# Kernel tuning notes

Measured on AMD Instinct MI355X. Metric: run time of the kernel, lower is better.

Reference implementation:

```python
import jax, jax.numpy as jnp
import numpy as np


def _bev_grid(theta, shift, H_out, W_out):
    # grid resolution in meters per output pixel (0.05 when H_out=800)
    gr = 0.05 * (800.0 / H_out)
    xs = -10.0 + gr / 2.0 + gr * jnp.arange(W_out, dtype=jnp.float32)   # [W]
    ys = 46.0 - gr / 2.0 - gr * jnp.arange(H_out, dtype=jnp.float32)    # [H]
    bx = jnp.broadcast_to(xs[None, :], (H_out, W_out))
    by = jnp.broadcast_to(ys[:, None], (H_out, W_out))
    base = jnp.stack([bx, by, jnp.ones((H_out, W_out), jnp.float32)], axis=-1)  # [H,W,3]
    # bmm(base.view(N,HW,3), theta^T) == einsum over last axis
    g = jnp.einsum('hwk,nik->nhwi', base, theta)  # [N,H,W,3]
    g = g / g[..., 2:3]
    gx = g[..., 0] / 608.0 - 1.0
    gy = (g[..., 1] - shift[:, None, None]) / 144.0 - 1.0
    return jnp.stack([gx, gy], axis=-1)  # [N,H,W,2]


def _grid_sample_bilinear_border(x, grid):
    # align_corners=False (torch default), padding_mode='border'
    N, C, Hin, Win = x.shape
    Hout, Wout = grid.shape[1], grid.shape[2]
    ix = ((grid[..., 0] + 1.0) * Win - 1.0) * 0.5
    iy = ((grid[..., 1] + 1.0) * Hin - 1.0) * 0.5
    ix0 = jnp.floor(ix)
    iy0 = jnp.floor(iy)
    wx = ix - ix0  # fractional weights
    wy = iy - iy0
    x0 = jnp.clip(ix0, 0, Win - 1).astype(jnp.int32)
    x1 = jnp.clip(ix0 + 1, 0, Win - 1).astype(jnp.int32)
    y0 = jnp.clip(iy0, 0, Hin - 1).astype(jnp.int32)
    y1 = jnp.clip(iy0 + 1, 0, Hin - 1).astype(jnp.int32)

    flat = x.reshape(N, C, Hin * Win)

    def gather(yi, xi):
        idx = (yi * Win + xi).reshape(N, 1, Hout * Wout)
        idx = jnp.broadcast_to(idx, (N, C, Hout * Wout))
        return jnp.take_along_axis(flat, idx, axis=2).reshape(N, C, Hout, Wout)

    v00 = gather(y0, x0)
    v01 = gather(y0, x1)
    v10 = gather(y1, x0)
    v11 = gather(y1, x1)
    wx = wx[:, None, :, :]
    wy = wy[:, None, :, :]
    return (v00 * (1 - wx) * (1 - wy) + v01 * wx * (1 - wy)
            + v10 * (1 - wx) * wy + v11 * wx * wy)


def setup_inputs() -> dict:
    key = jax.random.key(0)
    k1, k2, k3 = jax.random.split(key, 3)
    N, C, Hin, Win = 4, 16, 288, 1216
    x = jax.random.normal(k1, (N, C, Hin, Win), dtype=jnp.float32)
    # realistic homography: identity plus small perturbation
    theta = jnp.eye(3, dtype=jnp.float32)[None] + 0.1 * jax.random.normal(k2, (N, 3, 3), dtype=jnp.float32)
    shift = 10.0 * jax.random.uniform(k3, (N,), dtype=jnp.float32)
    return {"x": x, "theta": theta, "shift": shift, "H_out": 800, "W_out": 400}


def reference(x, theta, shift, H_out, W_out):
    grid = _bev_grid(theta, shift, H_out, W_out)
    return _grid_sample_bilinear_border(x, grid)
```

## Files before the change

kernel.cpp:

```cpp
#include <hip/hip_runtime.h>
#include <math.h>

constexpr int N    = 4;
constexpr int C    = 16;
constexpr int Hin  = 288;
constexpr int Win  = 1216;
constexpr int Hout = 800;
constexpr int Wout = 400;
constexpr int PIX_PER_N = Hout * Wout;
constexpr int CH_STRIDE = Hin * Win;

typedef float v2f __attribute__((ext_vector_type(2)));

constexpr double grd = 0.05 * (800.0 / (double)Hout);
constexpr float  GR  = (float)grd;
constexpr float  CX0 = (float)(-10.0 + grd / 2.0);
constexpr float  CY0 = (float)( 46.0 - grd / 2.0);

__device__ __forceinline__ float fbar(float x) {
    asm volatile("" : "+v"(x));
    return x;
}

struct Samp {
    int   lb0, lb1;
    bool  hi0, hi1, xpair;
    float w00, w01, w10, w11;
};

__device__ __forceinline__ Samp px_chain(int w, int h, const float* th, float shn) {
    float bx = CX0 + fbar(GR * (float)w);
    float by = CY0 - fbar(GR * (float)h);

    float t00 = th[0], t01 = th[1], t02 = th[2];
    float t10 = th[3], t11 = th[4], t12 = th[5];
    float t20 = th[6], t21 = th[7], t22 = th[8];

    float g0 = fbar(__builtin_fmaf(by, t01, fbar(bx * t00))) + t02;
    float g1 = fbar(__builtin_fmaf(by, t11, fbar(bx * t10))) + t12;
    float g2 = fbar(__builtin_fmaf(by, t21, fbar(bx * t20))) + t22;

    float p0 = g0 / g2;
    float p1 = g1 / g2;

    float gx = fbar(p0 / 608.0f) - 1.0f;
    float gy = fbar((p1 - shn) / 144.0f) - 1.0f;

    float ix = (fbar((gx + 1.0f) * (float)Win) - 1.0f) * 0.5f;
    float iy = (fbar((gy + 1.0f) * (float)Hin) - 1.0f) * 0.5f;

    float ix0f = floorf(ix);
    float iy0f = floorf(iy);
    float wx = ix - ix0f;
    float wy = iy - iy0f;

    int x0 = (int)fminf(fmaxf(ix0f,        0.0f), (float)(Win - 1));
    int x1 = (int)fminf(fmaxf(ix0f + 1.0f, 0.0f), (float)(Win - 1));
    int y0 = (int)fminf(fmaxf(iy0f,        0.0f), (float)(Hin - 1));
    int y1 = (int)fminf(fmaxf(iy0f + 1.0f, 0.0f), (float)(Hin - 1));

    float omwx = 1.0f - wx;
    float omwy = 1.0f - wy;

    Samp s;
    s.w00 = omwx * omwy;
    s.w01 = wx * omwy;
    s.w10 = omwx * wy;
    s.w11 = wx * wy;

    int lo0 = y0 * Win + x0;
    int lo1 = y1 * Win + x0;
    s.lb0 = min(lo0, CH_STRIDE - 2);
    s.lb1 = min(lo1, CH_STRIDE - 2);
    s.hi0 = lo0 > s.lb0;
    s.hi1 = lo1 > s.lb1;
    s.xpair = x1 > x0;
    return s;
}

__device__ __forceinline__ float combine(v2f r0, v2f r1, const Samp& s) {
    float v00 = s.hi0   ? r0.y : r0.x;
    float v01 = s.xpair ? r0.y : v00;
    float v10 = s.hi1   ? r1.y : r1.x;
    float v11 = s.xpair ? r1.y : v10;
    return v00 * s.w00 + v01 * s.w01 + v10 * s.w10 + v11 * s.w11;
}

__global__ __launch_bounds__(256) void bev_sample_kernel(
    const float* __restrict__ x,
    const float* __restrict__ theta,
    const float* __restrict__ shift,
    float* __restrict__ out)
{
    int tid2 = blockIdx.x * 256 + threadIdx.x;
    if (tid2 >= (N * Hout * Wout) / 2) return;
    int pid = tid2 * 2;

    int w = pid % Wout;
    int t = pid / Wout;
    int h = t % Hout;
    int n = t / Hout;

    const float* th  = theta + n * 9;
    const float  shn = shift[n];

    Samp sa = px_chain(w,     h, th, shn);
    Samp sb = px_chain(w + 1, h, th, shn);

    const float* xb = x + (size_t)n * C * CH_STRIDE;
    float* ob = out + ((size_t)(n * C) * Hout + h) * (size_t)Wout + w;

    #pragma unroll 1
    for (int half = 0; half < 2; ++half) {
        v2f r0a[8], r1a[8], r0b[8], r1b[8];
        #pragma unroll
        for (int j = 0; j < 8; ++j) {
            const float* pch = xb + (size_t)(half * 8 + j) * CH_STRIDE;
            r0a[j] = *reinterpret_cast<const v2f*>(pch + sa.lb0);
            r1a[j] = *reinterpret_cast<const v2f*>(pch + sa.lb1);
            r0b[j] = *reinterpret_cast<const v2f*>(pch + sb.lb0);
            r1b[j] = *reinterpret_cast<const v2f*>(pch + sb.lb1);
        }
        #pragma unroll
        for (int j = 0; j < 8; ++j) {
            v2f rr;
            rr.x = combine(r0a[j], r1a[j], sa);
            rr.y = combine(r0b[j], r1b[j], sb);
            __builtin_nontemporal_store(rr, reinterpret_cast<v2f*>(
                ob + (size_t)(half * 8 + j) * PIX_PER_N));
        }
    }
}

extern "C" void kernel_launch(void* const* d_in, const int* in_sizes, int n_in,
                              void* d_out, int out_size, void* d_ws, size_t ws_size,
                              hipStream_t stream) {
    const float* x     = (const float*)d_in[0];
    const float* theta = (const float*)d_in[1];
    const float* shift = (const float*)d_in[2];
    float* out = (float*)d_out;

    int total2 = (N * Hout * Wout) / 2;
    int blocks = (total2 + 255) / 256;
    bev_sample_kernel<<<blocks, 256, 0, stream>>>(x, theta, shift, out);
}
```

Before: 39.81 us.

## Assign each thread two distant pixels and issue all 64 gathers before combining

Each thread now handles pixel gid and pixel gid+TOTAL/2 instead of two adjacent pixels. All 16 channels for both pixels are loaded before any combine, which raises memory-level parallelism. Batch index reads use readfirstlane, relying on each wave sitting inside one batch, which holds because the pixels per batch are a multiple of 64. Adjacent lanes now load adjacent pixels, but stores become scalar float instead of float2, and register pressure rises.

```diff
diff --git a/kernel.cpp b/kernel.cpp
--- a/kernel.cpp
+++ b/kernel.cpp
@@ -9,8 +9,8 @@
 constexpr int Wout = 400;
 constexpr int PIX_PER_N = Hout * Wout;
 constexpr int CH_STRIDE = Hin * Win;
-
-typedef float v2f __attribute__((ext_vector_type(2)));
+constexpr int TOTAL = N * Hout * Wout;
+constexpr int HALF  = TOTAL / 2;
 
 constexpr double grd = 0.05 * (800.0 / (double)Hout);
 constexpr float  GR  = (float)grd;
@@ -78,7 +78,7 @@
     return s;
 }
 
-__device__ __forceinline__ float combine(v2f r0, v2f r1, const Samp& s) {
+__device__ __forceinline__ float combine(float2 r0, float2 r1, const Samp& s) {
     float v00 = s.hi0   ? r0.y : r0.x;
     float v01 = s.xpair ? r0.y : v00;
     float v10 = s.hi1   ? r1.y : r1.x;
@@ -92,43 +92,55 @@
     const float* __restrict__ shift,
     float* __restrict__ out)
 {
-    int tid2 = blockIdx.x * 256 + threadIdx.x;
-    if (tid2 >= (N * Hout * Wout) / 2) return;
-    int pid = tid2 * 2;
+    int gid = blockIdx.x * 256 + threadIdx.x;
 
-    int w = pid % Wout;
-    int t = pid / Wout;
-    int h = t % Hout;
-    int n = t / Hout;
+    int wA = gid % Wout;
+    int tA = gid / Wout;
+    int hA = tA % Hout;
+    int nA = tA / Hout;
+    int nAs = __builtin_amdgcn_readfirstlane(nA);
 
-    const float* th  = theta + n * 9;
-    const float  shn = shift[n];
+    Samp sA = px_chain(wA, hA, theta + nAs * 9, shift[nAs]);
+    const float* xbA = x + (size_t)nAs * C * CH_STRIDE;
 
-    Samp sa = px_chain(w,     h, th, shn);
-    Samp sb = px_chain(w + 1, h, th, shn);
+    float2 rA0[C], rA1[C];
+    #pragma unroll
+    for (int c = 0; c < C; ++c) {
+        const float* p = xbA + (size_t)c * CH_STRIDE;
+        rA0[c] = *reinterpret_cast<const float2*>(p + sA.lb0);
+        rA1[c] = *reinterpret_cast<const float2*>(p + sA.lb1);
+    }
 
-    const float* xb = x + (size_t)n * C * CH_STRIDE;
-    float* ob = out + ((size_t)(n * C) * Hout + h) * (size_t)Wout + w;
+    int pidB = gid + HALF;
+    int wB = pidB % Wout;
+    int tB = pidB / Wout;
+    int hB = tB % Hout;
+    int nB = tB / Hout;
+    int nBs = __builtin_amdgcn_readfirstlane(nB);
 
-    #pragma unroll 1
-    for (int half = 0; half < 2; ++half) {
-        v2f r0a[8], r1a[8], r0b[8], r1b[8];
-        #pragma unroll
-        for (int j = 0; j < 8; ++j) {
-            const float* pch = xb + (size_t)(half * 8 + j) * CH_STRIDE;
-            r0a[j] = *reinterpret_cast<const v2f*>(pch + sa.lb0);
-            r1a[j] = *reinterpret_cast<const v2f*>(pch + sa.lb1);
-            r0b[j] = *reinterpret_cast<const v2f*>(pch + sb.lb0);
-            r1b[j] = *reinterpret_cast<const v2f*>(pch + sb.lb1);
-        }
-        #pragma unroll
-        for (int j = 0; j < 8; ++j) {
-            v2f rr;
-            rr.x = combine(r0a[j], r1a[j], sa);
-            rr.y = combine(r0b[j], r1b[j], sb);
-            __builtin_nontemporal_store(rr, reinterpret_cast<v2f*>(
-                ob + (size_t)(half * 8 + j) * PIX_PER_N));
-        }
+    Samp sB = px_chain(wB, hB, theta + nBs * 9, shift[nBs]);
+    const float* xbB = x + (size_t)nBs * C * CH_STRIDE;
+
+    float2 rB0[C], rB1[C];
+    #pragma unroll
+    for (int c = 0; c < C; ++c) {
+        const float* p = xbB + (size_t)c * CH_STRIDE;
+        rB0[c] = *reinterpret_cast<const float2*>(p + sB.lb0);
+        rB1[c] = *reinterpret_cast<const float2*>(p + sB.lb1);
+    }
+
+    size_t obA = ((size_t)(nAs * C) * Hout + hA) * Wout + wA;
+    #pragma unroll
+    for (int c = 0; c < C; ++c) {
+        float r = combine(rA0[c], rA1[c], sA);
+        __builtin_nontemporal_store(r, &out[obA + (size_t)c * PIX_PER_N]);
+    }
+
+    size_t obB = ((size_t)(nBs * C) * Hout + hB) * Wout + wB;
+    #pragma unroll
+    for (int c = 0; c < C; ++c) {
+        float r = combine(rB0[c], rB1[c], sB);
+        __builtin_nontemporal_store(r, &out[obB + (size_t)c * PIX_PER_N]);
     }
 }
 
@@ -140,7 +152,6 @@
     const float* shift = (const float*)d_in[2];
     float* out = (float*)d_out;
 
-    int total2 = (N * Hout * Wout) / 2;
-    int blocks = (total2 + 255) / 256;
+    int blocks = HALF / 256;
     bev_sample_kernel<<<blocks, 256, 0, stream>>>(x, theta, shift, out);
 }
```

Measured after the change: 36.87 us (median of 2 runs). 1.08x faster.

## Process four pixels per thread with all 16 channels loaded at once

Applied to the files above, without the earlier changes.

Each thread now computes four adjacent output pixels instead of two and issues all 16 channels' gathers (128 float2 loads) before any combine, writing float4 nontemporal stores. This widens store vectors and exposes more memory-level parallelism per thread. The cost is much higher register pressure (256 floats of loads in flight) and a quarter as many threads, which lowers occupancy. The bounds check is dropped because the total divides evenly.

```diff
diff --git a/kernel.cpp b/kernel.cpp
--- a/kernel.cpp
+++ b/kernel.cpp
@@ -9,8 +9,9 @@
 constexpr int Wout = 400;
 constexpr int PIX_PER_N = Hout * Wout;
 constexpr int CH_STRIDE = Hin * Win;
+constexpr int TOTAL = N * Hout * Wout;
 
-typedef float v2f __attribute__((ext_vector_type(2)));
+typedef float v4f __attribute__((ext_vector_type(4)));
 
 constexpr double grd = 0.05 * (800.0 / (double)Hout);
 constexpr float  GR  = (float)grd;
@@ -78,7 +79,7 @@
     return s;
 }
 
-__device__ __forceinline__ float combine(v2f r0, v2f r1, const Samp& s) {
+__device__ __forceinline__ float combine(float2 r0, float2 r1, const Samp& s) {
     float v00 = s.hi0   ? r0.y : r0.x;
     float v01 = s.xpair ? r0.y : v00;
     float v10 = s.hi1   ? r1.y : r1.x;
@@ -92,43 +93,48 @@
     const float* __restrict__ shift,
     float* __restrict__ out)
 {
-    int tid2 = blockIdx.x * 256 + threadIdx.x;
-    if (tid2 >= (N * Hout * Wout) / 2) return;
-    int pid = tid2 * 2;
+    int tid4 = blockIdx.x * 256 + threadIdx.x;
+    int pid = tid4 * 4;
 
-    int w = pid % Wout;
-    int t = pid / Wout;
-    int h = t % Hout;
-    int n = t / Hout;
+    int w0 = pid % Wout;
+    int t  = pid / Wout;
+    int h  = t % Hout;
+    int n  = t / Hout;
 
     const float* th  = theta + n * 9;
     const float  shn = shift[n];
 
-    Samp sa = px_chain(w,     h, th, shn);
-    Samp sb = px_chain(w + 1, h, th, shn);
+    Samp s0 = px_chain(w0,     h, th, shn);
+    Samp s1 = px_chain(w0 + 1, h, th, shn);
+    Samp s2 = px_chain(w0 + 2, h, th, shn);
+    Samp s3 = px_chain(w0 + 3, h, th, shn);
 
     const float* xb = x + (size_t)n * C * CH_STRIDE;
-    float* ob = out + ((size_t)(n * C) * Hout + h) * (size_t)Wout + w;
 
-    #pragma unroll 1
-    for (int half = 0; half < 2; ++half) {
-        v2f r0a[8], r1a[8], r0b[8], r1b[8];
-        #pragma unroll
-        for (int j = 0; j < 8; ++j) {
-            const float* pch = xb + (size_t)(half * 8 + j) * CH_STRIDE;
-            r0a[j] = *reinterpret_cast<const v2f*>(pch + sa.lb0);
-            r1a[j] = *reinterpret_cast<const v2f*>(pch + sa.lb1);
-            r0b[j] = *reinterpret_cast<const v2f*>(pch + sb.lb0);
-            r1b[j] = *reinterpret_cast<const v2f*>(pch + sb.lb1);
-        }
-        #pragma unroll
-        for (int j = 0; j < 8; ++j) {
-            v2f rr;
-            rr.x = combine(r0a[j], r1a[j], sa);
-            rr.y = combine(r0b[j], r1b[j], sb);
-            __builtin_nontemporal_store(rr, reinterpret_cast<v2f*>(
-                ob + (size_t)(half * 8 + j) * PIX_PER_N));
-        }
+    float2 a0[C], a1[C], b0[C], b1[C], c0[C], c1[C], d0[C], d1[C];
+    #pragma unroll
+    for (int c = 0; c < C; ++c) {
+        const float* p = xb + (size_t)c * CH_STRIDE;
+        a0[c] = *reinterpret_cast<const float2*>(p + s0.lb0);
+        a1[c] = *reinterpret_cast<const float2*>(p + s0.lb1);
+        b0[c] = *reinterpret_cast<const float2*>(p + s1.lb0);
+        b1[c] = *reinterpret_cast<const float2*>(p + s1.lb1);
+        c0[c] = *reinterpret_cast<const float2*>(p + s2.lb0);
+        c1[c] = *reinterpret_cast<const float2*>(p + s2.lb1);
+        d0[c] = *reinterpret_cast<const float2*>(p + s3.lb0);
+        d1[c] = *reinterpret_cast<const float2*>(p + s3.lb1);
+    }
+
+    float* ob = out + ((size_t)(n * C) * Hout + h) * (size_t)Wout + w0;
+    #pragma unroll
+    for (int c = 0; c < C; ++c) {
+        v4f r;
+        r.x = combine(a0[c], a1[c], s0);
+        r.y = combine(b0[c], b1[c], s1);
+        r.z = combine(c0[c], c1[c], s2);
+        r.w = combine(d0[c], d1[c], s3);
+        __builtin_nontemporal_store(r, reinterpret_cast<v4f*>(
+            ob + (size_t)c * PIX_PER_N));
     }
 }
 
@@ -140,7 +146,6 @@
     const float* shift = (const float*)d_in[2];
     float* out = (float*)d_out;
 
-    int total2 = (N * Hout * Wout) / 2;
-    int blocks = (total2 + 255) / 256;
+    int blocks = (TOTAL / 4) / 256;
     bev_sample_kernel<<<blocks, 256, 0, stream>>>(x, theta, shift, out);
 }
```

After: 43.43 us. 9.1% more time.
